# Kernel optimization log

Measured on AMD Instinct MI355X. Metric: run time of the kernel, lower is better.

Reference implementation:

```python
import jax, jax.numpy as jnp
from jax import lax
import numpy as np

K = 4            # prototypes per class: 3 kmeans centroids + 1 backbone
EPS = 0.1        # sinkhorn entropic regularization
MAX_ITER = 100
THRESH = 0.01
KM_ITERS = 10    # Lloyd iterations (replaces host-side sklearn KMeans)
HW = 28          # the original reshapes pred to 28x28, fixing n = 784


def setup_inputs():
    key = jax.random.key(0)
    k1, k2, k3, k4 = jax.random.split(key, 4)
    b, n, d, c = 32, HW * HW, 1024, 20
    return {
        "query": jax.random.normal(k1, (b, n, d), dtype=jnp.float32),
        "score": jax.random.uniform(k2, (b, n, c), dtype=jnp.float32),
        "label": jax.random.randint(k3, (b, c), 0, 2),
        "gt": jax.random.randint(k4, (b, HW, HW), 0, c + 1),
        "weights": jnp.array([1.0, 1.0, 0.0, -1.0], dtype=jnp.float32),
    }


def _assign(dq, cen, selfm):
    # dq [b,m,d], cen [b,c,j,d], selfm [b,c,m] float mask -> one-hot labels, counts
    x2 = jnp.sum(dq * dq, axis=-1)                                   # [b,m]
    d2 = (x2[:, None, :, None]
          - 2.0 * jnp.einsum('bmd,bcjd->bcmj', dq, cen)
          + jnp.sum(cen * cen, axis=-1)[:, :, None, :])              # [b,c,m,j]
    oh = jax.nn.one_hot(jnp.argmin(d2, axis=-1), cen.shape[2], dtype=dq.dtype) * selfm[..., None]
    return oh, oh.sum(axis=2)


def _sinkhorn(Km, u, v):
    # vectorized over the [b,c] pair grid, per-pair early exit as in the torch loop
    def cond(st):
        it, r, cc, done = st
        return (it < MAX_ITER) & jnp.logical_not(jnp.all(done))

    def body(st):
        it, r, cc, done = st
        r1 = u / jnp.einsum('bcnj,bcj->bcn', Km, cc)
        c1 = v / jnp.einsum('bcnj,bcn->bcj', Km, r1)
        err = jnp.mean(jnp.abs(r1 - r), axis=-1)                     # [b,c]
        r = jnp.where(done[..., None], r, r1)
        cc = jnp.where(done[..., None], cc, c1)
        done = done | (err < THRESH)
        return it + 1, r, cc, done

    st = (jnp.int32(0), jnp.ones_like(u), jnp.ones_like(v),
          jnp.zeros(Km.shape[:2], dtype=bool))
    _, r, cc, _ = lax.while_loop(cond, body, st)
    return r[..., :, None] * cc[..., None, :] * Km                   # [b,c,n,K]


def _forward(query, score, label, gt, weights):
    b, n, d = query.shape
    c = score.shape[2]
    dq, ds = query[:, ::2, :], score[:, ::2, :]                      # stride-2 downsample
    m = dq.shape[1]
    cls_assign = jnp.argmax(ds, axis=-1)                             # [b,m]
    sel = cls_assign[:, None, :] == jnp.arange(c)[None, :, None]     # [b,c,m]
    selfm = sel.astype(query.dtype)
    cnt = selfm.sum(-1)                                              # [b,c]
    valid = (label > 0) & (cnt >= K)

    # ---- masked Lloyd's k-means with k-1 = 3 clusters per (image, class) pair
    order = jnp.argsort((~sel).astype(jnp.int32), axis=-1)           # masked points first
    init_idx = order[..., :K - 1]                                    # [b,c,3]
    cen = dq[jnp.arange(b)[:, None, None], init_idx]                 # [b,c,3,d]

    def km_step(cen, _):
        oh, kcnt = _assign(dq, cen, selfm)
        sums = jnp.einsum('bmd,bcmj->bcjd', dq, oh)
        cen = jnp.where(kcnt[..., None] > 0,
                        sums / jnp.maximum(kcnt, 1.0)[..., None], cen)
        return cen, None

    cen, _ = lax.scan(km_step, cen, None, length=KM_ITERS)
    oh, kcnt = _assign(dq, cen, selfm)                               # final labels

    # ---- sort centroids by mean cluster score (descending)
    sm = ds.mean(axis=-1)                                            # [b,m]
    avg = jnp.where(kcnt > 0,
                    jnp.einsum('bm,bcmj->bcj', sm, oh) / jnp.maximum(kcnt, 1.0),
                    -jnp.inf)
    ordj = jnp.argsort(-avg, axis=-1)                                # [b,c,3]
    cen = jnp.take_along_axis(cen, ordj[..., None], axis=2)

    # ---- backbone prototype = mean over unselected downsampled tokens
    un = 1.0 - selfm
    backbone = jnp.einsum('bmd,bcm->bcd', dq, un) / jnp.maximum(m - cnt, 1.0)[..., None]
    protos = jnp.concatenate([cen, backbone[:, :, None, :]], axis=2)  # [b,c,4,d]

    # ---- OT between query[0] tokens and the 4 prototypes (original uses query[0] always)
    q0 = query[0]
    q0h = q0 / jnp.maximum(jnp.linalg.norm(q0, axis=-1, keepdims=True), 1e-12)
    ph = protos / jnp.maximum(jnp.linalg.norm(protos, axis=-1, keepdims=True), 1e-12)
    sim = jnp.einsum('nd,bcjd->bcnj', q0h, ph)                       # [b,c,n,4]
    Km = lax.stop_gradient(jnp.exp(-(1.0 - sim) / EPS))              # torch.no_grad
    u = jnp.full((b, c, n), 1.0 / n, dtype=query.dtype)
    v = jnp.full((b, c, K), 1.0 / K, dtype=query.dtype)
    T = lax.stop_gradient(_sinkhorn(Km, u, v))                       # [b,c,n,4]

    valid = valid & jnp.logical_not(jnp.any(jnp.isnan(T), axis=(2, 3)))
    pred = jnp.einsum('bcnj,j->bcn', T, weights)                     # [b,c,n]

    # ---- BCE vs gt masks (28x28 -> 28x28 bilinear resize is the identity)
    y = (gt.reshape(b, -1)[:, None, :] == (jnp.arange(c) + 1)[None, :, None]).astype(pred.dtype)
    p = jnp.clip(pred, 0.0, 1.0)
    bce = -(y * jnp.maximum(jnp.log(p), -100.0)
            + (1.0 - y) * jnp.maximum(jnp.log(1.0 - p), -100.0)).mean(axis=-1)  # [b,c]
    bce = jnp.where(valid, bce, 0.0)
    total_n = valid.sum().astype(pred.dtype)
    return bce.sum() / (total_n + 1e-4)


def reference(query, score, label, gt, weights):
    return _forward(query, score, label, gt, weights)
```

## Files before the change

kernel.cpp:

```cpp
#include <hip/hip_runtime.h>
#include <cmath>

#define BB 32
#define NN 784
#define MM 392
#define DD 1024
#define CC 20
#define JJ 3
#define KP 4
#define KM_ITERS 10
#define GMAX 64
#define NCOL (BB * CC * KP)
#define NQ0B 98
#define NTSB (BB * 16)

typedef __attribute__((ext_vector_type(8))) short bf16x8;
typedef __attribute__((ext_vector_type(4))) float f32x4;

__device__ inline unsigned short f2bf(float x) {
  unsigned int u = __float_as_uint(x);
  u += 0x7FFFu + ((u >> 16) & 1u);
  return (unsigned short)(u >> 16);
}
__device__ inline float bf2f(unsigned short h) {
  return __uint_as_float(((unsigned int)h) << 16);
}
__device__ inline void f2bf2(float x, unsigned short& hi, unsigned short& lo) {
  hi = f2bf(x);
  lo = f2bf(x - bf2f(hi));
}
__device__ inline void store_bf4(unsigned short* baseh, unsigned short* basel,
                                 int idx4, float4 v) {
  ushort4 h, l;
  f2bf2(v.x, h.x, l.x); f2bf2(v.y, h.y, l.y);
  f2bf2(v.z, h.z, l.z); f2bf2(v.w, h.w, l.w);
  ((ushort4*)baseh)[idx4] = h;
  ((ushort4*)basel)[idx4] = l;
}

__global__ __launch_bounds__(512) void k_prep(
    const float* __restrict__ score, const float* __restrict__ query,
    const int* __restrict__ label,
    int* __restrict__ cls, float* __restrict__ sm, int* __restrict__ valid,
    float* __restrict__ totalsum,
    unsigned short* __restrict__ q0hh, unsigned short* __restrict__ q0hl,
    float* __restrict__ gred) {
  int blk = blockIdx.x;
  int tid = threadIdx.x, lane = tid & 63, wv = tid >> 6;
  __shared__ int s_cnt[CC];
  __shared__ float sa[8][64];

  if (blk < BB) {
    int b = blk;
    if (tid < CC) s_cnt[tid] = 0;
    __syncthreads();
    if (tid < MM) {
      const float4* s4 = (const float4*)(score + ((size_t)b * NN + 2 * tid) * CC);
      float4 r[5];
      #pragma unroll
      for (int k = 0; k < 5; k++) r[k] = s4[k];
      const float* s = (const float*)r;
      float best = s[0]; int bi = 0; float acc = s[0];
      #pragma unroll
      for (int c = 1; c < CC; c++) { float v = s[c]; acc += v; if (v > best) { best = v; bi = c; } }
      cls[b * MM + tid] = bi;
      sm[b * MM + tid] = acc / (float)CC;
      atomicAdd(&s_cnt[bi], 1);
    }
    __syncthreads();
    if (tid < CC) {
      int cv = s_cnt[tid];
      valid[b * CC + tid] = (label[b * CC + tid] > 0 && cv >= KP) ? 1 : 0;
    }
    if (blk == 0 && tid == 0) { gred[0] = 0.f; gred[1] = 0.f; ((int*)gred)[2] = 0; }
  } else if (blk < BB + NQ0B) {
    int n = (blk - BB) * 8 + wv;
    const float* src = query + (size_t)n * DD;
    float v[16];
    float ss = 0.f;
    #pragma unroll
    for (int j = 0; j < 16; j++) { v[j] = src[lane + 64 * j]; ss += v[j] * v[j]; }
    #pragma unroll
    for (int o = 32; o > 0; o >>= 1) ss += __shfl_xor(ss, o, 64);
    float nrm = fmaxf(sqrtf(ss), 1e-12f);
    #pragma unroll
    for (int j = 0; j < 16; j++) {
      unsigned short hi, lo;
      f2bf2(v[j] / nrm, hi, lo);
      q0hh[(size_t)n * DD + lane + 64 * j] = hi;
      q0hl[(size_t)n * DD + lane + 64 * j] = lo;
    }
  } else {
    int t = blk - BB - NQ0B;
    int b = t >> 4, ch = t & 15;
    const float* qb = query + (size_t)b * NN * DD + ch * 64 + lane;
    float a = 0.f;
    #pragma unroll 7
    for (int r = 0; r < 49; r++) {
      int i = wv * 49 + r;
      a += qb[(size_t)(2 * i) * DD];
    }
    sa[wv][lane] = a;
    __syncthreads();
    if (wv == 0) {
      float s = 0.f;
      #pragma unroll
      for (int w = 0; w < 8; w++) s += sa[w][lane];
      totalsum[(size_t)b * DD + ch * 64 + lane] = s;
    }
  }
}

__global__ __launch_bounds__(512) void k_gram(
    const float* __restrict__ query, const int* __restrict__ cls,
    const int* __restrict__ valid, const float* __restrict__ sm,
    const float* __restrict__ totalsum,
    unsigned short* __restrict__ phh, unsigned short* __restrict__ phl) {
  int bc = blockIdx.x;
  if (!valid[bc]) return;
  int b = bc / CC, c = bc - b * CC;
  int tid = threadIdx.x, lane = tid & 63, wv = tid >> 6;
  const float* qb = query + (size_t)b * NN * DD;
  __shared__ int s_wtot[8];
  __shared__ int s_list[GMAX];
  __shared__ __align__(16) float Xs[GMAX][128];
  __shared__ float Gl[GMAX][65];
  __shared__ float s_w[JJ][GMAX];
  __shared__ int s_rank[JJ];
  __shared__ float s_red2[8];

  int flag = 0;
  if (tid < MM) flag = (cls[b * MM + tid] == c) ? 1 : 0;
  unsigned long long msk = __ballot(flag);
  int wp = __popcll(msk & ((1ull << lane) - 1ull));
  if (lane == 0) s_wtot[wv] = __popcll(msk);
  __syncthreads();
  int off = 0, mtot = 0;
  #pragma unroll
  for (int w = 0; w < 8; w++) { int t = s_wtot[w]; if (w < wv) off += t; mtot += t; }
  int mc = mtot > GMAX ? GMAX : mtot;
  if (flag) { int pos = off + wp; if (pos < GMAX) s_list[pos] = tid; }
  __syncthreads();

  const float* pb[4] = {nullptr, nullptr, nullptr, nullptr};
  float* xd[4] = {nullptr, nullptr, nullptr, nullptr};
  #pragma unroll
  for (int s = 0; s < 4; s++) {
    int e = tid + s * 512;
    if (e < mc * 32) {
      int row = e >> 5, f = e & 31;
      pb[s] = qb + (size_t)(2 * s_list[row]) * DD + f * 4;
      xd[s] = &Xs[row][4 * (f ^ ((row >> 2) & 7))];
    }
  }

  int T = (mc + 3) >> 2;
  int ntile = T * (T + 1) / 2;
  int ti = -1, tj = 0;
  float a[4][4] = {};
  if (tid < ntile) {
    int p = tid;
    int i = (int)floorf((sqrtf(8.0f * (float)p + 1.0f) - 1.0f) * 0.5f);
    while ((i + 1) * (i + 2) / 2 <= p) i++;
    while (i * (i + 1) / 2 > p) i--;
    ti = i; tj = p - i * (i + 1) / 2;
  }

  float4 cur[4], nxt[4];
  #pragma unroll
  for (int s = 0; s < 4; s++) {
    cur[s] = make_float4(0.f, 0.f, 0.f, 0.f);
    nxt[s] = make_float4(0.f, 0.f, 0.f, 0.f);
    if (pb[s]) cur[s] = *(const float4*)(pb[s]);
  }
  for (int ch = 0; ch < 8; ch++) {
    __syncthreads();
    #pragma unroll
    for (int s = 0; s < 4; s++) if (pb[s]) *(float4*)xd[s] = cur[s];
    if (ch < 7) {
      #pragma unroll
      for (int s = 0; s < 4; s++) if (pb[s]) nxt[s] = *(const float4*)(pb[s] + (ch + 1) * 128);
    }
    __syncthreads();
    if (ti >= 0) {
      int su = ti & 7, sw = tj & 7;
      const float4* xr0 = (const float4*)&Xs[4 * ti + 0][0];
      const float4* xr1 = (const float4*)&Xs[4 * ti + 1][0];
      const float4* xr2 = (const float4*)&Xs[4 * ti + 2][0];
      const float4* xr3 = (const float4*)&Xs[4 * ti + 3][0];
      const float4* xc0 = (const float4*)&Xs[4 * tj + 0][0];
      const float4* xc1 = (const float4*)&Xs[4 * tj + 1][0];
      const float4* xc2 = (const float4*)&Xs[4 * tj + 2][0];
      const float4* xc3 = (const float4*)&Xs[4 * tj + 3][0];
      #pragma unroll 8
      for (int kk = 0; kk < 32; kk++) {
        int ku = kk ^ su, kw = kk ^ sw;
        float4 u[4], w[4];
        u[0] = xr0[ku]; u[1] = xr1[ku]; u[2] = xr2[ku]; u[3] = xr3[ku];
        w[0] = xc0[kw]; w[1] = xc1[kw]; w[2] = xc2[kw]; w[3] = xc3[kw];
        #pragma unroll
        for (int r = 0; r < 4; r++)
          #pragma unroll
          for (int cq = 0; cq < 4; cq++)
            a[r][cq] += u[r].x * w[cq].x + u[r].y * w[cq].y
                      + u[r].z * w[cq].z + u[r].w * w[cq].w;
      }
    }
    #pragma unroll
    for (int s = 0; s < 4; s++) cur[s] = nxt[s];
  }

  if (ti >= 0) {
    #pragma unroll
    for (int r = 0; r < 4; r++) {
      int gr = 4 * ti + r;
      if (gr < mc) {
        #pragma unroll
        for (int cq = 0; cq < 4; cq++) {
          int gc = 4 * tj + cq;
          if (gc < mc) { Gl[gr][gc] = a[r][cq]; Gl[gc][gr] = a[r][cq]; }
        }
      }
    }
  }
  __syncthreads();

  if (wv == 0) {
    bool act = lane < mc;
    float smv = act ? sm[b * MM + s_list[lane]] : 0.f;
    s_w[0][lane] = (lane == 0) ? 1.f : 0.f;
    s_w[1][lane] = (lane == 1) ? 1.f : 0.f;
    s_w[2][lane] = (lane == 2) ? 1.f : 0.f;
    int aj = 0, n0 = 0, n1 = 0, n2 = 0;
    for (int it = 0; it <= KM_ITERS; it++) {
      float h0 = 0.f, h1 = 0.f, h2 = 0.f;
      if (act) {
        for (int i = 0; i < mc; i++) {
          float g = Gl[lane][i];
          h0 += s_w[0][i] * g; h1 += s_w[1][i] * g; h2 += s_w[2][i] * g;
        }
      }
      float t0 = s_w[0][lane] * h0, t1 = s_w[1][lane] * h1, t2 = s_w[2][lane] * h2;
      for (int o = 1; o < 64; o <<= 1) {
        t0 += __shfl_xor(t0, o, 64); t1 += __shfl_xor(t1, o, 64); t2 += __shfl_xor(t2, o, 64);
      }
      float e0 = t0 - 2.f * h0, e1 = t1 - 2.f * h1, e2 = t2 - 2.f * h2;
      aj = 0; float bv = e0;
      if (e1 < bv) { bv = e1; aj = 1; }
      if (e2 < bv) { bv = e2; aj = 2; }
      n0 = __popcll(__ballot(act && aj == 0));
      n1 = __popcll(__ballot(act && aj == 1));
      n2 = __popcll(__ballot(act && aj == 2));
      if (it == KM_ITERS) break;
      if (act) {
        if (n0 > 0) s_w[0][lane] = (aj == 0) ? 1.f / (float)n0 : 0.f;
        if (n1 > 0) s_w[1][lane] = (aj == 1) ? 1.f / (float)n1 : 0.f;
        if (n2 > 0) s_w[2][lane] = (aj == 2) ? 1.f / (float)n2 : 0.f;
      }
    }
    float s0 = (act && aj == 0) ? smv : 0.f;
    float s1 = (act && aj == 1) ? smv : 0.f;
    float s2 = (act && aj == 2) ? smv : 0.f;
    for (int o = 1; o < 64; o <<= 1) {
      s0 += __shfl_xor(s0, o, 64); s1 += __shfl_xor(s1, o, 64); s2 += __shfl_xor(s2, o, 64);
    }
    if (lane == 0) {
      float avg[JJ];
      avg[0] = (n0 > 0) ? s0 / (float)n0 : -INFINITY;
      avg[1] = (n1 > 0) ? s1 / (float)n1 : -INFINITY;
      avg[2] = (n2 > 0) ? s2 / (float)n2 : -INFINITY;
      bool used[JJ] = {false, false, false};
      for (int s = 0; s < JJ; s++) {
        int bi = -1; float bv = 0.f;
        for (int j = 0; j < JJ; j++)
          if (!used[j] && (bi < 0 || avg[j] > bv)) { bi = j; bv = avg[j]; }
        used[bi] = true; s_rank[bi] = s;
      }
    }
  }
  __syncthreads();

  float4 a0 = make_float4(0.f, 0.f, 0.f, 0.f), a1 = make_float4(0.f, 0.f, 0.f, 0.f);
  int j = tid >> 7, q = tid & 127;
  if (j < 3) {
    for (int g = 0; g < mc; g++) {
      float w = s_w[j][g];
      if (w != 0.f) {
        const float4* row = (const float4*)(qb + (size_t)(2 * s_list[g]) * DD);
        float4 v0 = row[q], v1 = row[q + 128];
        a0.x += w * v0.x; a0.y += w * v0.y; a0.z += w * v0.z; a0.w += w * v0.w;
        a1.x += w * v1.x; a1.y += w * v1.y; a1.z += w * v1.z; a1.w += w * v1.w;
      }
    }
  } else {
    for (int g = 0; g < mc; g++) {
      const float4* row = (const float4*)(qb + (size_t)(2 * s_list[g]) * DD);
      float4 v0 = row[q], v1 = row[q + 128];
      a0.x += v0.x; a0.y += v0.y; a0.z += v0.z; a0.w += v0.w;
      a1.x += v1.x; a1.y += v1.y; a1.z += v1.z; a1.w += v1.w;
    }
    const float4* tb = (const float4*)(totalsum + (size_t)b * DD);
    float4 t0 = tb[q], t1 = tb[q + 128];
    float denom = fmaxf((float)(MM - mtot), 1.f);
    float inv = 1.f / denom;
    a0.x = (t0.x - a0.x) * inv; a0.y = (t0.y - a0.y) * inv;
    a0.z = (t0.z - a0.z) * inv; a0.w = (t0.w - a0.w) * inv;
    a1.x = (t1.x - a1.x) * inv; a1.y = (t1.y - a1.y) * inv;
    a1.z = (t1.z - a1.z) * inv; a1.w = (t1.w - a1.w) * inv;
  }
  float ssq = a0.x * a0.x + a0.y * a0.y + a0.z * a0.z + a0.w * a0.w
            + a1.x * a1.x + a1.y * a1.y + a1.z * a1.z + a1.w * a1.w;
  #pragma unroll
  for (int o = 1; o < 64; o <<= 1) ssq += __shfl_xor(ssq, o, 64);
  if (lane == 0) s_red2[wv] = ssq;
  __syncthreads();
  float nrm = fmaxf(sqrtf(s_red2[2 * j] + s_red2[2 * j + 1]), 1e-12f);
  int prow = (j < 3) ? s_rank[j] : 3;
  size_t rowoff = ((size_t)bc * KP + prow) * DD;
  float4 o0 = make_float4(a0.x / nrm, a0.y / nrm, a0.z / nrm, a0.w / nrm);
  float4 o1 = make_float4(a1.x / nrm, a1.y / nrm, a1.z / nrm, a1.w / nrm);
  store_bf4(phh + rowoff, phl + rowoff, q, o0);
  store_bf4(phh + rowoff, phl + rowoff, q + 128, o1);
}

__global__ __launch_bounds__(64) void k_gemm(
    const unsigned short* __restrict__ Ah, const unsigned short* __restrict__ Al,
    const unsigned short* __restrict__ Bh, const unsigned short* __restrict__ Bl,
    float* __restrict__ P) {
  int n0 = blockIdx.y * 64;
  int m0 = blockIdx.x * 64;
  int lane = threadIdx.x;
  int kh = lane >> 4;
  int lr = lane & 15;

  const unsigned short* pa_h[4]; const unsigned short* pa_l[4];
  #pragma unroll
  for (int mi = 0; mi < 4; mi++) {
    size_t o = (size_t)(m0 + mi * 16 + lr) * DD + kh * 8;
    pa_h[mi] = Ah + o; pa_l[mi] = Al + o;
  }
  const unsigned short* pb_h[4]; const unsigned short* pb_l[4];
  #pragma unroll
  for (int ni = 0; ni < 4; ni++) {
    int col = n0 + ni * 16 + lr;
    size_t o = (size_t)col * DD + kh * 8;
    pb_h[ni] = Bh + o; pb_l[ni] = Bl + o;
  }

  f32x4 acc[4][4];
  #pragma unroll
  for (int mi = 0; mi < 4; mi++)
    #pragma unroll
    for (int ni = 0; ni < 4; ni++) acc[mi][ni] = (f32x4){0.f, 0.f, 0.f, 0.f};

  for (int k0 = 0; k0 < DD; k0 += 32) {
    bf16x8 ah[4], al[4], bh[4], bl[4];
    #pragma unroll
    for (int i = 0; i < 4; i++) {
      ah[i] = *(const bf16x8*)(pa_h[i] + k0);
      al[i] = *(const bf16x8*)(pa_l[i] + k0);
      bh[i] = *(const bf16x8*)(pb_h[i] + k0);
      bl[i] = *(const bf16x8*)(pb_l[i] + k0);
    }
    #pragma unroll
    for (int mi = 0; mi < 4; mi++)
      #pragma unroll
      for (int ni = 0; ni < 4; ni++) {
        acc[mi][ni] = __builtin_amdgcn_mfma_f32_16x16x32_bf16(ah[mi], bh[ni], acc[mi][ni], 0, 0, 0);
        acc[mi][ni] = __builtin_amdgcn_mfma_f32_16x16x32_bf16(ah[mi], bl[ni], acc[mi][ni], 0, 0, 0);
        acc[mi][ni] = __builtin_amdgcn_mfma_f32_16x16x32_bf16(al[mi], bh[ni], acc[mi][ni], 0, 0, 0);
      }
  }

  #pragma unroll
  for (int ni = 0; ni < 4; ni++) {
    int col = n0 + ni * 16 + lr;
    #pragma unroll
    for (int mi = 0; mi < 4; mi++) {
      int m = m0 + mi * 16 + kh * 4;
      if (m < NN) {
        *(f32x4*)(P + (size_t)col * NN + m) = acc[mi][ni];
      }
    }
  }
}

__global__ __launch_bounds__(256) void k_sink(const float* __restrict__ P,
    const int* __restrict__ valid, const int* __restrict__ gt,
    const float* __restrict__ wts, float* __restrict__ gred, float* __restrict__ out) {
  int wv = threadIdx.x >> 6, lane = threadIdx.x & 63;
  int bc = blockIdx.x * 4 + wv;
  int b = bc / CC, c = bc - b * CC;
  float bce_out = 0.f; int vld_out = 0;

  if (valid[bc]) {
    float4 kv[13]; float rr[13];
    #pragma unroll
    for (int s = 0; s < 13; s++) {
      int n = lane + 64 * s;
      kv[s] = make_float4(0.f, 0.f, 0.f, 0.f); rr[s] = 1.f;
      if (n < NN) {
        float4 o;
        o.x = expf(-(1.0f - P[((size_t)(4 * bc + 0)) * NN + n]) / 0.1f);
        o.y = expf(-(1.0f - P[((size_t)(4 * bc + 1)) * NN + n]) / 0.1f);
        o.z = expf(-(1.0f - P[((size_t)(4 * bc + 2)) * NN + n]) / 0.1f);
        o.w = expf(-(1.0f - P[((size_t)(4 * bc + 3)) * NN + n]) / 0.1f);
        kv[s] = o;
      }
    }
    const float uu = 1.0f / (float)NN, vv = 1.0f / (float)KP;
    float c0 = 1.f, c1 = 1.f, c2 = 1.f, c3 = 1.f;
    for (int it = 0; it < 100; it++) {
      float dsum = 0.f, p0 = 0.f, p1 = 0.f, p2 = 0.f, p3 = 0.f;
      #pragma unroll
      for (int s = 0; s < 13; s++) {
        int n = lane + 64 * s;
        if (n < NN) {
          float4 k4 = kv[s];
          float S = k4.x * c0 + k4.y * c1 + k4.z * c2 + k4.w * c3;
          float r1 = uu / S;
          dsum += fabsf(r1 - rr[s]);
          rr[s] = r1;
          p0 += k4.x * r1; p1 += k4.y * r1; p2 += k4.z * r1; p3 += k4.w * r1;
        }
      }
      #pragma unroll
      for (int o = 1; o < 64; o <<= 1) {
        dsum += __shfl_xor(dsum, o, 64);
        p0 += __shfl_xor(p0, o, 64); p1 += __shfl_xor(p1, o, 64);
        p2 += __shfl_xor(p2, o, 64); p3 += __shfl_xor(p3, o, 64);
      }
      c0 = vv / p0; c1 = vv / p1; c2 = vv / p2; c3 = vv / p3;
      if (dsum / (float)NN < 0.01f) break;
    }
    float w0 = wts[0], w1 = wts[1], w2 = wts[2], w3 = wts[3];
    float bsum = 0.f; int nanloc = 0;
    const int* gtb = gt + b * NN;
    #pragma unroll
    for (int s = 0; s < 13; s++) {
      int n = lane + 64 * s;
      if (n < NN) {
        float4 k4 = kv[s];
        float rv = rr[s];
        float T0 = rv * c0 * k4.x, T1 = rv * c1 * k4.y, T2 = rv * c2 * k4.z, T3 = rv * c3 * k4.w;
        if (T0 != T0 || T1 != T1 || T2 != T2 || T3 != T3) nanloc = 1;
        float pred = T0 * w0 + T1 * w1 + T2 * w2 + T3 * w3;
        float pcl = fminf(fmaxf(pred, 0.f), 1.f);
        float t = (gtb[n] == c + 1) ? fmaxf(logf(pcl), -100.f) : fmaxf(logf(1.f - pcl), -100.f);
        bsum += t;
      }
    }
    #pragma unroll
    for (int o = 1; o < 64; o <<= 1) bsum += __shfl_xor(bsum, o, 64);
    int nanany = __any(nanloc);
    if (!nanany) { bce_out = -(bsum / (float)NN); vld_out = 1; }
  }

  if (lane == 0) {
    if (vld_out) { atomicAdd(&gred[0], bce_out); atomicAdd(&gred[1], 1.f); }
    __threadfence();
    int old = atomicAdd((int*)gred + 2, 1);
    if (old == BB * CC - 1) {
      float s = atomicAdd(&gred[0], 0.f);
      float n2 = atomicAdd(&gred[1], 0.f);
      out[0] = s / (n2 + 0.0001f);
    }
  }
}

extern "C" void kernel_launch(void* const* d_in, const int* in_sizes, int n_in,
                              void* d_out, int out_size, void* d_ws, size_t ws_size,
                              hipStream_t stream) {
  (void)in_sizes; (void)n_in; (void)out_size; (void)ws_size;
  const float* query = (const float*)d_in[0];
  const float* score = (const float*)d_in[1];
  const int*   label = (const int*)d_in[2];
  const int*   gt    = (const int*)d_in[3];
  const float* wts   = (const float*)d_in[4];
  float* ws = (float*)d_ws;

  size_t off = 0;
  int* cls = (int*)(ws + off);            off += (size_t)BB * MM;
  float* sm = ws + off;                   off += (size_t)BB * MM;
  int* valid = (int*)(ws + off);          off += (size_t)BB * CC;
  float* totalsum = ws + off;             off += (size_t)BB * DD;
  unsigned short* q0hh = (unsigned short*)(ws + off);  off += (size_t)NN * DD / 2;
  unsigned short* q0hl = (unsigned short*)(ws + off);  off += (size_t)NN * DD / 2;
  unsigned short* phh = (unsigned short*)(ws + off);   off += (size_t)BB * CC * KP * DD / 2;
  unsigned short* phl = (unsigned short*)(ws + off);   off += (size_t)BB * CC * KP * DD / 2;
  float* P = ws + off;                    off += (size_t)NCOL * NN;
  float* gred = ws + off;                 off += 16;

  k_prep<<<BB + NQ0B + NTSB, 512, 0, stream>>>(score, query, label, cls, sm, valid,
                                               totalsum, q0hh, q0hl, gred);
  k_gram<<<BB * CC, 512, 0, stream>>>(query, cls, valid, sm, totalsum, phh, phl);
  dim3 gg((NN + 63) / 64, NCOL / 64);
  k_gemm<<<gg, 64, 0, stream>>>(q0hh, q0hl, phh, phl, P);
  k_sink<<<160, 256, 0, stream>>>(P, valid, gt, wts, gred, (float*)d_out);
}
```

Baseline: 315.5 us.

## Compute per-class Gram matrix with split-bf16 MFMA instead of scalar FP32 FMAs

The Gram matrix of selected query rows in k_gram is now built with 16x16x32 bf16 MFMA instructions, one wave per 16x16 lower-triangular tile, using a hi/lo bf16 split (three products) to approximate FP32 accuracy. Rows are converted to bf16 hi/lo pairs when staged into padded LDS buffers, and padding rows are zeroed. This replaces the per-thread 4x4 scalar FMA tiling, cutting ALU work in the Gram step. The cost is conversion overhead, extra LDS, and slightly reduced precision versus full FP32, which could flip kmeans assignments.

```diff
diff --git a/kernel.cpp b/kernel.cpp
--- a/kernel.cpp
+++ b/kernel.cpp
@@ -123,7 +123,8 @@
   const float* qb = query + (size_t)b * NN * DD;
   __shared__ int s_wtot[8];
   __shared__ int s_list[GMAX];
-  __shared__ __align__(16) float Xs[GMAX][128];
+  __shared__ __align__(16) unsigned short Xh[GMAX][136];
+  __shared__ __align__(16) unsigned short Xl[GMAX][136];
   __shared__ float Gl[GMAX][65];
   __shared__ float s_w[JJ][GMAX];
   __shared__ int s_rank[JJ];
@@ -142,29 +143,44 @@
   if (flag) { int pos = off + wp; if (pos < GMAX) s_list[pos] = tid; }
   __syncthreads();
 
+  int T16 = (mc + 15) >> 4;
+  int ntile16 = T16 * (T16 + 1) / 2;
+
+  int zrows = 16 * T16 - mc;
+  for (int z = tid; z < zrows * 34; z += 512) {
+    int zr = mc + z / 34, zc = (z % 34) * 4;
+    ushort4 zz = {0, 0, 0, 0};
+    *(ushort4*)&Xh[zr][zc] = zz;
+    *(ushort4*)&Xl[zr][zc] = zz;
+  }
+
   const float* pb[4] = {nullptr, nullptr, nullptr, nullptr};
-  float* xd[4] = {nullptr, nullptr, nullptr, nullptr};
+  unsigned short* xdh[4]; unsigned short* xdl[4];
   #pragma unroll
   for (int s = 0; s < 4; s++) {
     int e = tid + s * 512;
     if (e < mc * 32) {
       int row = e >> 5, f = e & 31;
       pb[s] = qb + (size_t)(2 * s_list[row]) * DD + f * 4;
-      xd[s] = &Xs[row][4 * (f ^ ((row >> 2) & 7))];
-    }
-  }
-
-  int T = (mc + 3) >> 2;
-  int ntile = T * (T + 1) / 2;
-  int ti = -1, tj = 0;
-  float a[4][4] = {};
-  if (tid < ntile) {
-    int p = tid;
-    int i = (int)floorf((sqrtf(8.0f * (float)p + 1.0f) - 1.0f) * 0.5f);
-    while ((i + 1) * (i + 2) / 2 <= p) i++;
-    while (i * (i + 1) / 2 > p) i--;
-    ti = i; tj = p - i * (i + 1) / 2;
-  }
+      xdh[s] = &Xh[row][f * 4];
+      xdl[s] = &Xl[row][f * 4];
+    }
+  }
+
+  int ti0 = -1, tj0 = 0, ti1 = -1, tj1 = 0;
+  if (wv < ntile16) {
+    int t = wv, i = 0;
+    while ((i + 1) * (i + 2) / 2 <= t) i++;
+    ti0 = i; tj0 = t - i * (i + 1) / 2;
+  }
+  if (wv + 8 < ntile16) {
+    int t = wv + 8, i = 0;
+    while ((i + 1) * (i + 2) / 2 <= t) i++;
+    ti1 = i; tj1 = t - i * (i + 1) / 2;
+  }
+  f32x4 acc0 = (f32x4){0.f, 0.f, 0.f, 0.f};
+  f32x4 acc1 = (f32x4){0.f, 0.f, 0.f, 0.f};
+  int fr = lane & 15, fk = (lane >> 4) * 8;
 
   float4 cur[4], nxt[4];
   #pragma unroll
@@ -176,51 +192,70 @@
   for (int ch = 0; ch < 8; ch++) {
     __syncthreads();
     #pragma unroll
-    for (int s = 0; s < 4; s++) if (pb[s]) *(float4*)xd[s] = cur[s];
+    for (int s = 0; s < 4; s++) {
+      if (pb[s]) {
+        ushort4 h, l;
+        f2bf2(cur[s].x, h.x, l.x); f2bf2(cur[s].y, h.y, l.y);
+        f2bf2(cur[s].z, h.z, l.z); f2bf2(cur[s].w, h.w, l.w);
+        *(ushort4*)xdh[s] = h;
+        *(ushort4*)xdl[s] = l;
+      }
+    }
     if (ch < 7) {
       #pragma unroll
       for (int s = 0; s < 4; s++) if (pb[s]) nxt[s] = *(const float4*)(pb[s] + (ch + 1) * 128);
     }
     __syncthreads();
-    if (ti >= 0) {
-      int su = ti & 7, sw = tj & 7;
-      const float4* xr0 = (const float4*)&Xs[4 * ti + 0][0];
-      const float4* xr1 = (const float4*)&Xs[4 * ti + 1][0];
-      const float4* xr2 = (const float4*)&Xs[4 * ti + 2][0];
-      const float4* xr3 = (const float4*)&Xs[4 * ti + 3][0];
-      const float4* xc0 = (const float4*)&Xs[4 * tj + 0][0];
-      const float4* xc1 = (const float4*)&Xs[4 * tj + 1][0];
-      const float4* xc2 = (const float4*)&Xs[4 * tj + 2][0];
-      const float4* xc3 = (const float4*)&Xs[4 * tj + 3][0];
-      #pragma unroll 8
-      for (int kk = 0; kk < 32; kk++) {
-        int ku = kk ^ su, kw = kk ^ sw;
-        float4 u[4], w[4];
-        u[0] = xr0[ku]; u[1] = xr1[ku]; u[2] = xr2[ku]; u[3] = xr3[ku];
-        w[0] = xc0[kw]; w[1] = xc1[kw]; w[2] = xc2[kw]; w[3] = xc3[kw];
-        #pragma unroll
-        for (int r = 0; r < 4; r++)
-          #pragma unroll
-          for (int cq = 0; cq < 4; cq++)
-            a[r][cq] += u[r].x * w[cq].x + u[r].y * w[cq].y
-                      + u[r].z * w[cq].z + u[r].w * w[cq].w;
+    if (ti0 >= 0) {
+      const unsigned short* pah = &Xh[16 * ti0 + fr][fk];
+      const unsigned short* pal = &Xl[16 * ti0 + fr][fk];
+      const unsigned short* pbh = &Xh[16 * tj0 + fr][fk];
+      const unsigned short* pbl = &Xl[16 * tj0 + fr][fk];
+      #pragma unroll
+      for (int ks = 0; ks < 4; ks++) {
+        bf16x8 ah = *(const bf16x8*)(pah + 32 * ks);
+        bf16x8 al = *(const bf16x8*)(pal + 32 * ks);
+        bf16x8 bh = *(const bf16x8*)(pbh + 32 * ks);
+        bf16x8 bl = *(const bf16x8*)(pbl + 32 * ks);
+        acc0 = __builtin_amdgcn_mfma_f32_16x16x32_bf16(ah, bh, acc0, 0, 0, 0);
+        acc0 = __builtin_amdgcn_mfma_f32_16x16x32_bf16(ah, bl, acc0, 0, 0, 0);
+        acc0 = __builtin_amdgcn_mfma_f32_16x16x32_bf16(al, bh, acc0, 0, 0, 0);
+      }
+    }
+    if (ti1 >= 0) {
+      const unsigned short* pah = &Xh[16 * ti1 + fr][fk];
+      const unsigned short* pal = &Xl[16 * ti1 + fr][fk];
+      const unsigned short* pbh = &Xh[16 * tj1 + fr][fk];
+      const unsigned short* pbl = &Xl[16 * tj1 + fr][fk];
+      #pragma unroll
+      for (int ks = 0; ks < 4; ks++) {
+        bf16x8 ah = *(const bf16x8*)(pah + 32 * ks);
+        bf16x8 al = *(const bf16x8*)(pal + 32 * ks);
+        bf16x8 bh = *(const bf16x8*)(pbh + 32 * ks);
+        bf16x8 bl = *(const bf16x8*)(pbl + 32 * ks);
+        acc1 = __builtin_amdgcn_mfma_f32_16x16x32_bf16(ah, bh, acc1, 0, 0, 0);
+        acc1 = __builtin_amdgcn_mfma_f32_16x16x32_bf16(ah, bl, acc1, 0, 0, 0);
+        acc1 = __builtin_amdgcn_mfma_f32_16x16x32_bf16(al, bh, acc1, 0, 0, 0);
       }
     }
     #pragma unroll
     for (int s = 0; s < 4; s++) cur[s] = nxt[s];
   }
 
-  if (ti >= 0) {
+  if (ti0 >= 0) {
     #pragma unroll
     for (int r = 0; r < 4; r++) {
-      int gr = 4 * ti + r;
-      if (gr < mc) {
-        #pragma unroll
-        for (int cq = 0; cq < 4; cq++) {
-          int gc = 4 * tj + cq;
-          if (gc < mc) { Gl[gr][gc] = a[r][cq]; Gl[gc][gr] = a[r][cq]; }
-        }
-      }
+      int gr = 16 * ti0 + (lane >> 4) * 4 + r;
+      int gc = 16 * tj0 + fr;
+      Gl[gr][gc] = acc0[r]; Gl[gc][gr] = acc0[r];
+    }
+  }
+  if (ti1 >= 0) {
+    #pragma unroll
+    for (int r = 0; r < 4; r++) {
+      int gr = 16 * ti1 + (lane >> 4) * 4 + r;
+      int gc = 16 * tj1 + fr;
+      Gl[gr][gc] = acc1[r]; Gl[gc][gr] = acc1[r];
     }
   }
   __syncthreads();
```

After: 261.9 us. 17.0% less time.
